# Optimization experiments

Hardware: AMD Instinct MI355X
Metric: run time of the kernel (lower is better)

## Reference

```python
import jax, jax.numpy as jnp
import numpy as np

BATCH = 32
ROW_DIM = 8192
COL_DIM = 8192
N_BLOCKS = 512
ROW_BS = ROW_DIM // N_BLOCKS  # 16
COL_BS = COL_DIM // N_BLOCKS  # 16


def setup_inputs() -> dict:
    key = jax.random.key(0)
    k1, k2 = jax.random.split(key)
    x = jax.random.normal(k1, (BATCH, COL_DIM), dtype=jnp.float32)
    # xavier-uniform-ish init scale for blocks [n_blocks, p, q]
    limit = np.sqrt(6.0 / (ROW_BS + COL_BS))
    blocks = jax.random.uniform(k2, (N_BLOCKS, ROW_BS, COL_BS), dtype=jnp.float32,
                                minval=-limit, maxval=limit)
    return {"x": x, "blocks": blocks}


def reference(x, blocks):
    b = x.shape[0]
    n, p, q = blocks.shape
    x_blocks = x.reshape(b, n, q)  # [B, n, q]
    # circulant index pattern: block (i, j) uses blocks[(i - j) % n]
    idx = (jnp.arange(n)[:, None] - jnp.arange(n)[None, :]) % n  # [n, n]
    blocks_shifted = blocks[idx]  # [n, n, p, q] -- the gather-expand intermediate
    y_blocks = jnp.einsum('mnpq,bnq->bmp', blocks_shifted, x_blocks)  # [B, n, p]
    return y_blocks.reshape(b, n * p)
```

## Files before the change

kernel.cpp:

```cpp
#include <hip/hip_runtime.h>
#include <hip/hip_bf16.h>

#define DIM 8192

typedef __bf16 bf16x8 __attribute__((ext_vector_type(8)));
typedef __bf16 bf16x2 __attribute__((ext_vector_type(2)));
typedef float f32x4 __attribute__((ext_vector_type(4)));
typedef float f32x2 __attribute__((ext_vector_type(2)));

__device__ __forceinline__ uint2 cvt_f4(const float4 v) {
  bf16x2 lo = __builtin_convertvector((f32x2){v.x, v.y}, bf16x2);
  bf16x2 hi = __builtin_convertvector((f32x2){v.z, v.w}, bf16x2);
  uint2 r;
  r.x = __builtin_bit_cast(unsigned, lo);
  r.y = __builtin_bit_cast(unsigned, hi);
  return r;
}

#define GL2LDS(gp, lp)                                                        \
  __builtin_amdgcn_global_load_lds(                                           \
      (const __attribute__((address_space(1))) void*)(gp),                    \
      (__attribute__((address_space(3))) void*)(lp), 16, 0, 0)

__global__ __launch_bounds__(256)
void bcl_prep_kernel(const float* __restrict__ X, const float* __restrict__ Blk,
                     unsigned short* __restrict__ Xp, unsigned short* __restrict__ Wp,
                     float4* __restrict__ Out) {
  const int T = blockIdx.x * 256 + threadIdx.x;
  if (T < 32768) {
    const int c  = T;
    const int p  = c & 15;
    const int kh = (c >> 4) & 3;
    const int b0 = (c >> 6) & 1;
    const int s  = (c >> 7) & 15;
    const int kc = c >> 11;
    const float* src = X + (b0 * 16 + p) * DIM + kc * 512 + s * 32 +
                       ((kh >> 1) << 4) + ((kh & 1) << 3);
    const float4 v0 = reinterpret_cast<const float4*>(src)[0];
    const float4 v1 = reinterpret_cast<const float4*>(src)[1];
    const uint2 a = cvt_f4(v0), b = cvt_f4(v1);
    uint4 o; o.x = a.x; o.y = a.y; o.z = b.x; o.w = b.y;
    *reinterpret_cast<uint4*>(Xp + c * 8) = o;
  } else if (T < 49152) {
    const int b  = T - 32768;
    const int d  = b >> 5;
    const int q5 = b & 31;
    const int p  = q5 & 15;
    const int qh = q5 >> 4;
    const float* src = Blk + d * 256 + p * 16 + qh * 8;
    const float4 v0 = reinterpret_cast<const float4*>(src)[0];
    const float4 v1 = reinterpret_cast<const float4*>(src)[1];
    const uint2 a = cvt_f4(v0), bb = cvt_f4(v1);
    uint4 o; o.x = a.x; o.y = a.y; o.z = bb.x; o.w = bb.y;
    *reinterpret_cast<uint4*>(Wp + b * 8) = o;
  } else {
    const int z = T - 49152;
    const float4 zero = {0.f, 0.f, 0.f, 0.f};
    #pragma unroll
    for (int i = 0; i < 4; ++i) Out[z * 4 + i] = zero;
  }
}

__global__ __launch_bounds__(512, 4)
void bcl_mfma_kernel(const unsigned short* __restrict__ Xp,
                     const unsigned short* __restrict__ Wp,
                     float* __restrict__ Out) {
  __shared__ __align__(16) unsigned short Xl[16384];
  __shared__ __align__(16) unsigned short Wl[48 * 256];

  const int tid  = threadIdx.x;
  const int lane = tid & 63;
  const int wid  = tid >> 6;
  const int mc   = blockIdx.x & 31;
  const int kc   = blockIdx.x >> 5;

  const char* xsrc = reinterpret_cast<const char*>(Xp + kc * 16384);
  #pragma unroll
  for (int ro = 0; ro < 4; ++ro) {
    const int lb = ro * 8192 + wid * 1024;
    GL2LDS(xsrc + lb + lane * 16, reinterpret_cast<char*>(Xl) + lb);
  }

  const int dbase = (mc * 16 - kc * 32 - 31) & 511;
  const char* wsrc = reinterpret_cast<const char*>(Wp);
  #pragma unroll
  for (int ro = 0; ro < 3; ++ro) {
    const int lb = ro * 8192 + wid * 1024;
    const int B  = lb + lane * 16;
    const int w  = B >> 9;
    const int d  = (dbase + w) & 511;
    GL2LDS(wsrc + d * 512 + (B & 511), reinterpret_cast<char*>(Wl) + lb);
  }

  __syncthreads();

  const unsigned short* Xb = &Xl[lane << 3];
  const unsigned short* Wb = &Wl[(((lane >> 5) ^ 1) << 8) + (((lane >> 4) & 1) << 7) + ((lane & 15) << 3)];

  f32x4 acc[2][2];
  #pragma unroll
  for (int t = 0; t < 2; ++t)
    #pragma unroll
    for (int b = 0; b < 2; ++b)
      acc[t][b] = (f32x4){0.f, 0.f, 0.f, 0.f};

  #pragma unroll 4
  for (int s = 0; s < 16; ++s) {
    const bf16x8 x0 = *reinterpret_cast<const bf16x8*>(Xb + (s << 10));
    const bf16x8 x1 = *reinterpret_cast<const bf16x8*>(Xb + (s << 10) + 512);
    #pragma unroll
    for (int t = 0; t < 2; ++t) {
      const int mt = (wid << 1) + t;
      const bf16x8 wf = *reinterpret_cast<const bf16x8*>(Wb + ((mt + 30 - 2 * s) << 8));
      acc[t][0] = __builtin_amdgcn_mfma_f32_16x16x32_bf16(x0, wf, acc[t][0], 0, 0, 0);
      acc[t][1] = __builtin_amdgcn_mfma_f32_16x16x32_bf16(x1, wf, acc[t][1], 0, 0, 0);
    }
  }

  float* outp = Out + mc * 256;
  #pragma unroll
  for (int t = 0; t < 2; ++t) {
    const int col = ((wid << 1) + t) * 16 + (lane & 15);
    #pragma unroll
    for (int b0 = 0; b0 < 2; ++b0) {
      const int brow = b0 * 16 + ((lane >> 4) << 2);
      #pragma unroll
      for (int r = 0; r < 4; ++r)
        atomicAdd(outp + (brow + r) * DIM + col, acc[t][b0][r]);
    }
  }
}

extern "C" void kernel_launch(void* const* d_in, const int* in_sizes, int n_in,
                              void* d_out, int out_size, void* d_ws, size_t ws_size,
                              hipStream_t stream) {
  const float* X   = (const float*)d_in[0];
  const float* Blk = (const float*)d_in[1];
  unsigned short* Xp = (unsigned short*)d_ws;
  unsigned short* Wp = Xp + 262144;
  float* Out = (float*)d_out;

  bcl_prep_kernel<<<dim3(256), dim3(256), 0, stream>>>(X, Blk, Xp, Wp, (float4*)Out);
  bcl_mfma_kernel<<<dim3(512), dim3(512), 0, stream>>>(Xp, Wp, Out);
}
```

Before: 71.95 us.

## Replace atomic split-K accumulation with partial buffers and a separate reduce kernel

The output zeroing in the prep kernel and the float atomicAdds in the MFMA kernel are removed. Each of the 16 K-chunks now writes its partial tile to its own workspace slice, and a new reduce kernel sums the 16 slices into the output. This avoids atomic contention and the zero-fill pass. In exchange it adds a third kernel launch and about 16 MB of extra partial-sum writes and reads.

```diff
diff --git a/kernel.cpp b/kernel.cpp
--- a/kernel.cpp
+++ b/kernel.cpp
@@ -2,6 +2,8 @@
 #include <hip/hip_bf16.h>
 
 #define DIM 8192
+#define KSPLIT 16
+#define PARTIAL_ELEMS (32 * DIM)
 
 typedef __bf16 bf16x8 __attribute__((ext_vector_type(8)));
 typedef __bf16 bf16x2 __attribute__((ext_vector_type(2)));
@@ -24,8 +26,7 @@
 
 __global__ __launch_bounds__(256)
 void bcl_prep_kernel(const float* __restrict__ X, const float* __restrict__ Blk,
-                     unsigned short* __restrict__ Xp, unsigned short* __restrict__ Wp,
-                     float4* __restrict__ Out) {
+                     unsigned short* __restrict__ Xp, unsigned short* __restrict__ Wp) {
   const int T = blockIdx.x * 256 + threadIdx.x;
   if (T < 32768) {
     const int c  = T;
@@ -41,7 +42,7 @@
     const uint2 a = cvt_f4(v0), b = cvt_f4(v1);
     uint4 o; o.x = a.x; o.y = a.y; o.z = b.x; o.w = b.y;
     *reinterpret_cast<uint4*>(Xp + c * 8) = o;
-  } else if (T < 49152) {
+  } else {
     const int b  = T - 32768;
     const int d  = b >> 5;
     const int q5 = b & 31;
@@ -53,18 +54,13 @@
     const uint2 a = cvt_f4(v0), bb = cvt_f4(v1);
     uint4 o; o.x = a.x; o.y = a.y; o.z = bb.x; o.w = bb.y;
     *reinterpret_cast<uint4*>(Wp + b * 8) = o;
-  } else {
-    const int z = T - 49152;
-    const float4 zero = {0.f, 0.f, 0.f, 0.f};
-    #pragma unroll
-    for (int i = 0; i < 4; ++i) Out[z * 4 + i] = zero;
   }
 }
 
 __global__ __launch_bounds__(512, 4)
 void bcl_mfma_kernel(const unsigned short* __restrict__ Xp,
                      const unsigned short* __restrict__ Wp,
-                     float* __restrict__ Out) {
+                     float* __restrict__ Ws) {
   __shared__ __align__(16) unsigned short Xl[16384];
   __shared__ __align__(16) unsigned short Wl[48 * 256];
 
@@ -117,7 +113,7 @@
     }
   }
 
-  float* outp = Out + mc * 256;
+  float* base = Ws + (size_t)kc * PARTIAL_ELEMS + mc * 256;
   #pragma unroll
   for (int t = 0; t < 2; ++t) {
     const int col = ((wid << 1) + t) * 16 + (lane & 15);
@@ -126,9 +122,21 @@
       const int brow = b0 * 16 + ((lane >> 4) << 2);
       #pragma unroll
       for (int r = 0; r < 4; ++r)
-        atomicAdd(outp + (brow + r) * DIM + col, acc[t][b0][r]);
+        base[(brow + r) * DIM + col] = acc[t][b0][r];
     }
   }
+}
+
+__global__ __launch_bounds__(256)
+void bcl_reduce_kernel(const float4* __restrict__ Ws, float4* __restrict__ Out) {
+  const int f = blockIdx.x * 256 + threadIdx.x;
+  float4 a = Ws[f];
+  #pragma unroll
+  for (int kc = 1; kc < KSPLIT; ++kc) {
+    const float4 v = Ws[kc * (PARTIAL_ELEMS / 4) + f];
+    a.x += v.x; a.y += v.y; a.z += v.z; a.w += v.w;
+  }
+  Out[f] = a;
 }
 
 extern "C" void kernel_launch(void* const* d_in, const int* in_sizes, int n_in,
@@ -138,8 +146,11 @@
   const float* Blk = (const float*)d_in[1];
   unsigned short* Xp = (unsigned short*)d_ws;
   unsigned short* Wp = Xp + 262144;
+  float* Ws  = (float*)(Wp + 131072);
   float* Out = (float*)d_out;
 
-  bcl_prep_kernel<<<dim3(256), dim3(256), 0, stream>>>(X, Blk, Xp, Wp, (float4*)Out);
-  bcl_mfma_kernel<<<dim3(512), dim3(512), 0, stream>>>(Xp, Wp, Out);
+  bcl_prep_kernel<<<dim3(192), dim3(256), 0, stream>>>(X, Blk, Xp, Wp);
+  bcl_mfma_kernel<<<dim3(512), dim3(512), 0, stream>>>(Xp, Wp, Ws);
+  bcl_reduce_kernel<<<dim3(PARTIAL_ELEMS / 4 / 256), dim3(256), 0, stream>>>(
+      (const float4*)Ws, (float4*)Out);
 }
```

Result: no change. 71.72 us (-0.3%).

## Replace split-K atomics with full-K per-block loop and in-LDS wave reduction

Applied to the files above, without the earlier changes.

The MFMA kernel is restructured so each block owns a 64-column by 16-batch output tile and loops over all K in 32 double-buffered stages. The eight waves split K and combine their partials in LDS instead of using global atomicAdd, so the output no longer needs zeroing in the prep kernel. The X repack layout changes to match. This removes atomic traffic and the zero-fill pass, but leaves each block with a long serial loop, one barrier per stage and fewer blocks (256).

```diff
diff --git a/kernel.cpp b/kernel.cpp
--- a/kernel.cpp
+++ b/kernel.cpp
@@ -24,110 +24,114 @@
 
 __global__ __launch_bounds__(256)
 void bcl_prep_kernel(const float* __restrict__ X, const float* __restrict__ Blk,
-                     unsigned short* __restrict__ Xp, unsigned short* __restrict__ Wp,
-                     float4* __restrict__ Out) {
+                     unsigned short* __restrict__ Xp, unsigned short* __restrict__ Wp) {
   const int T = blockIdx.x * 256 + threadIdx.x;
   if (T < 32768) {
-    const int c  = T;
-    const int p  = c & 15;
-    const int kh = (c >> 4) & 3;
-    const int b0 = (c >> 6) & 1;
-    const int s  = (c >> 7) & 15;
-    const int kc = c >> 11;
-    const float* src = X + (b0 * 16 + p) * DIM + kc * 512 + s * 32 +
+    const int p  = T & 15;
+    const int kh = (T >> 4) & 3;
+    const int sw = (T >> 6) & 7;
+    const int h  = (T >> 9) & 31;
+    const int b0 = (T >> 14) & 1;
+    const float* src = X + (b0 * 16 + p) * DIM + h * 256 + sw * 32 +
                        ((kh >> 1) << 4) + ((kh & 1) << 3);
     const float4 v0 = reinterpret_cast<const float4*>(src)[0];
     const float4 v1 = reinterpret_cast<const float4*>(src)[1];
     const uint2 a = cvt_f4(v0), b = cvt_f4(v1);
     uint4 o; o.x = a.x; o.y = a.y; o.z = b.x; o.w = b.y;
-    *reinterpret_cast<uint4*>(Xp + c * 8) = o;
-  } else if (T < 49152) {
+    *reinterpret_cast<uint4*>(Xp + T * 8) = o;
+  } else {
     const int b  = T - 32768;
     const int d  = b >> 5;
-    const int q5 = b & 31;
-    const int p  = q5 & 15;
-    const int qh = q5 >> 4;
+    const int p  = b & 15;
+    const int qh = (b >> 4) & 1;
     const float* src = Blk + d * 256 + p * 16 + qh * 8;
     const float4 v0 = reinterpret_cast<const float4*>(src)[0];
     const float4 v1 = reinterpret_cast<const float4*>(src)[1];
     const uint2 a = cvt_f4(v0), bb = cvt_f4(v1);
     uint4 o; o.x = a.x; o.y = a.y; o.z = bb.x; o.w = bb.y;
     *reinterpret_cast<uint4*>(Wp + b * 8) = o;
-  } else {
-    const int z = T - 49152;
-    const float4 zero = {0.f, 0.f, 0.f, 0.f};
-    #pragma unroll
-    for (int i = 0; i < 4; ++i) Out[z * 4 + i] = zero;
   }
 }
 
-__global__ __launch_bounds__(512, 4)
-void bcl_mfma_kernel(const unsigned short* __restrict__ Xp,
+__global__ __launch_bounds__(512)
+void bcl_mono_kernel(const unsigned short* __restrict__ Xp,
                      const unsigned short* __restrict__ Wp,
                      float* __restrict__ Out) {
-  __shared__ __align__(16) unsigned short Xl[16384];
-  __shared__ __align__(16) unsigned short Wl[48 * 256];
+  __shared__ __align__(16) unsigned short LDSB[18432];
 
   const int tid  = threadIdx.x;
   const int lane = tid & 63;
   const int wid  = tid >> 6;
-  const int mc   = blockIdx.x & 31;
-  const int kc   = blockIdx.x >> 5;
+  const int b0   = blockIdx.x & 1;
+  const int cg   = blockIdx.x >> 1;
+  const int i0   = cg << 2;
 
-  const char* xsrc = reinterpret_cast<const char*>(Xp + kc * 16384);
+  const char* xsrc = reinterpret_cast<const char*>(Xp) + (size_t)(b0 * 32) * 8192;
+  const char* wsrc = reinterpret_cast<const char*>(Wp);
+  char* Xl = reinterpret_cast<char*>(LDSB);
+  char* Wl = reinterpret_cast<char*>(LDSB) + 16384;
+
+  auto STAGE = [&](int h, int buf) {
+    const int dbase = (i0 - (h << 4) - 15) & 511;
+    for (int t = wid; t < 18; t += 8) {
+      if (t < 8) {
+        const int lb = t << 10;
+        GL2LDS(xsrc + h * 8192 + lb + lane * 16, Xl + buf * 8192 + lb);
+      } else {
+        const int lb = (t - 8) << 10;
+        const int B  = lb + lane * 16;
+        const int w  = B >> 9;
+        const int d  = (dbase + w) & 511;
+        GL2LDS(wsrc + d * 512 + (B & 511), Wl + buf * 10240 + lb);
+      }
+    }
+  };
+
+  f32x4 acc[4];
   #pragma unroll
-  for (int ro = 0; ro < 4; ++ro) {
-    const int lb = ro * 8192 + wid * 1024;
-    GL2LDS(xsrc + lb + lane * 16, reinterpret_cast<char*>(Xl) + lb);
+  for (int mt = 0; mt < 4; ++mt) acc[mt] = (f32x4){0.f, 0.f, 0.f, 0.f};
+
+  const int xoff = (wid << 10) + (lane << 4);
+  const int woff = ((((lane >> 5) ^ 1) << 8) + (((lane >> 4) & 1) << 7) +
+                    ((lane & 15) << 3)) * 2;
+
+  STAGE(0, 0);
+  __syncthreads();
+
+  #pragma unroll 1
+  for (int h = 0; h < 32; ++h) {
+    const int buf = h & 1;
+    if (h < 31) STAGE(h + 1, buf ^ 1);
+    const bf16x8 xv = *reinterpret_cast<const bf16x8*>(Xl + buf * 8192 + xoff);
+    const char* wb = Wl + buf * 10240 + woff;
+    #pragma unroll
+    for (int mt = 0; mt < 4; ++mt) {
+      const bf16x8 wf = *reinterpret_cast<const bf16x8*>(wb + ((mt + 14 - (wid << 1)) << 9));
+      acc[mt] = __builtin_amdgcn_mfma_f32_16x16x32_bf16(xv, wf, acc[mt], 0, 0, 0);
+    }
+    __syncthreads();
   }
 
-  const int dbase = (mc * 16 - kc * 32 - 31) & 511;
-  const char* wsrc = reinterpret_cast<const char*>(Wp);
+  float* red = reinterpret_cast<float*>(LDSB);
   #pragma unroll
-  for (int ro = 0; ro < 3; ++ro) {
-    const int lb = ro * 8192 + wid * 1024;
-    const int B  = lb + lane * 16;
-    const int w  = B >> 9;
-    const int d  = (dbase + w) & 511;
-    GL2LDS(wsrc + d * 512 + (B & 511), reinterpret_cast<char*>(Wl) + lb);
+  for (int mt = 0; mt < 4; ++mt) {
+    const int ebase = (wid << 10) + (mt << 8) + (((lane >> 4) << 2) << 4) + (lane & 15);
+    #pragma unroll
+    for (int r = 0; r < 4; ++r)
+      red[ebase + (r << 4)] = acc[mt][r];
   }
-
   __syncthreads();
 
-  const unsigned short* Xb = &Xl[lane << 3];
-  const unsigned short* Wb = &Wl[(((lane >> 5) ^ 1) << 8) + (((lane >> 4) & 1) << 7) + ((lane & 15) << 3)];
-
-  f32x4 acc[2][2];
   #pragma unroll
-  for (int t = 0; t < 2; ++t)
+  for (int e = tid; e < 1024; e += 512) {
+    float s = 0.f;
     #pragma unroll
-    for (int b = 0; b < 2; ++b)
-      acc[t][b] = (f32x4){0.f, 0.f, 0.f, 0.f};
-
-  #pragma unroll 4
-  for (int s = 0; s < 16; ++s) {
-    const bf16x8 x0 = *reinterpret_cast<const bf16x8*>(Xb + (s << 10));
-    const bf16x8 x1 = *reinterpret_cast<const bf16x8*>(Xb + (s << 10) + 512);
-    #pragma unroll
-    for (int t = 0; t < 2; ++t) {
-      const int mt = (wid << 1) + t;
-      const bf16x8 wf = *reinterpret_cast<const bf16x8*>(Wb + ((mt + 30 - 2 * s) << 8));
-      acc[t][0] = __builtin_amdgcn_mfma_f32_16x16x32_bf16(x0, wf, acc[t][0], 0, 0, 0);
-      acc[t][1] = __builtin_amdgcn_mfma_f32_16x16x32_bf16(x1, wf, acc[t][1], 0, 0, 0);
-    }
-  }
-
-  float* outp = Out + mc * 256;
-  #pragma unroll
-  for (int t = 0; t < 2; ++t) {
-    const int col = ((wid << 1) + t) * 16 + (lane & 15);
-    #pragma unroll
-    for (int b0 = 0; b0 < 2; ++b0) {
-      const int brow = b0 * 16 + ((lane >> 4) << 2);
-      #pragma unroll
-      for (int r = 0; r < 4; ++r)
-        atomicAdd(outp + (brow + r) * DIM + col, acc[t][b0][r]);
-    }
+    for (int sw = 0; sw < 8; ++sw) s += red[(sw << 10) + e];
+    const int mt  = e >> 8;
+    const int el  = e & 255;
+    const int r16 = el >> 4;
+    const int c16 = el & 15;
+    Out[(b0 * 16 + r16) * DIM + (cg << 6) + (mt << 4) + c16] = s;
   }
 }
 
@@ -140,6 +144,6 @@
   unsigned short* Wp = Xp + 262144;
   float* Out = (float*)d_out;
 
-  bcl_prep_kernel<<<dim3(256), dim3(256), 0, stream>>>(X, Blk, Xp, Wp, (float4*)Out);
-  bcl_mfma_kernel<<<dim3(512), dim3(512), 0, stream>>>(Xp, Wp, Out);
+  bcl_prep_kernel<<<dim3(192), dim3(256), 0, stream>>>(X, Blk, Xp, Wp);
+  bcl_mono_kernel<<<dim3(256), dim3(512), 0, stream>>>(Xp, Wp, Out);
 }
```

After: 73.67 us. 1.02x slower.
